# Kernel optimization log

Hardware: AMD Instinct MI355X
Metric: run time of the kernel (lower is better)

Reference implementation:

```python
import jax, jax.numpy as jnp
import numpy as np

D_STATE = 128   # Mamba2 default (the SS2D d_state=16 is never forwarded to Mamba2)
N_HEADS = 4     # d_ssm // headdim = d_model / (d_model//4)
D_CONV = 4
EPS = 1e-5


def silu(v):
    return v * jax.nn.sigmoid(v)


def setup_inputs() -> dict:
    key = jax.random.key(0)
    ks = jax.random.split(key, 12)
    d_model = 256
    d_inner = 2 * d_model            # expand=2
    d_ssm = d_model
    conv_dim = d_ssm + 2 * D_STATE   # 512
    d_in_proj = 2 * d_inner + 2 * D_STATE + N_HEADS  # 1284
    B, H, W = 8, 64, 64
    inp = {
        "x": jax.random.normal(ks[0], (B, d_model, H, W), jnp.float32),
        "in_proj_w": jax.random.normal(ks[1], (d_in_proj, d_model), jnp.float32) * 0.02,
        "conv_w": jax.random.normal(ks[2], (conv_dim, D_CONV), jnp.float32) * 0.2,
        "conv_b": jnp.zeros((conv_dim,), jnp.float32),
        "dt_bias": jax.random.normal(ks[3], (N_HEADS,), jnp.float32) * 0.1,
        "A_log": jnp.log(jax.random.uniform(ks[4], (N_HEADS,), jnp.float32, 1.0, 16.0)),
        "D": jax.random.normal(ks[5], (N_HEADS,), jnp.float32),
        "norm_w": jnp.ones((d_ssm,), jnp.float32),
        "out_proj_w": jax.random.normal(ks[6], (d_model, d_inner), jnp.float32) * 0.02,
        "se_w1": jax.random.normal(ks[7], (d_model // 4, d_model), jnp.float32) * 0.05,
        "se_b1": jnp.zeros((d_model // 4,), jnp.float32),
        "se_w2": jax.random.normal(ks[8], (d_model, d_model // 4), jnp.float32) * 0.05,
        "se_b2": jnp.zeros((d_model,), jnp.float32),
    }
    return inp


def _forward(x, in_proj_w, conv_w, conv_b, dt_bias, A_log, D, norm_w,
             out_proj_w, se_w1, se_b1, se_w2, se_b2):
    Bb, C, H, W = x.shape
    L = H * W
    d_model = C
    d_inner = 2 * d_model
    d_ssm = d_model
    d_mlp = d_inner - d_ssm
    headdim = d_ssm // N_HEADS
    conv_dim = d_ssm + 2 * D_STATE

    u = x.reshape(Bb, C, L).transpose(0, 2, 1)              # (b, l, c)
    zxbcdt = u @ in_proj_w.T                                 # (b, l, 1284)
    z0 = zxbcdt[..., :d_mlp]
    x0 = zxbcdt[..., d_mlp:2 * d_mlp]
    z = zxbcdt[..., 2 * d_mlp:2 * d_mlp + d_ssm]
    xBC = zxbcdt[..., 2 * d_mlp + d_ssm:2 * d_mlp + d_ssm + conv_dim]
    dt = zxbcdt[..., -N_HEADS:]

    dt = jax.nn.softplus(dt + dt_bias)                       # (b, l, h)

    # causal depthwise conv along l, kernel size D_CONV
    xpad = jnp.pad(xBC, ((0, 0), (D_CONV - 1, 0), (0, 0)))
    xconv = conv_b
    for k in range(D_CONV):
        xconv = xconv + xpad[:, k:k + L, :] * conv_w[:, k]
    xconv = silu(xconv)

    xs = xconv[..., :d_ssm]
    Bm = xconv[..., d_ssm:d_ssm + D_STATE]                   # (b, l, n) ngroups=1
    Cm = xconv[..., d_ssm + D_STATE:]                        # (b, l, n)
    xh = xs.reshape(Bb, L, N_HEADS, headdim)                 # (b, l, h, p)

    A = -jnp.exp(A_log)                                      # (h,)

    def step(hstate, inp):
        xt, dtt, Bt, Ct = inp  # (b,h,p), (b,h), (b,n), (b,n)
        dA = jnp.exp(dtt * A)                                # (b, h)
        hstate = hstate * dA[:, :, None, None] + \
            (dtt[:, :, None, None] * xt[..., None]) * Bt[:, None, None, :]
        y = jnp.einsum('bhpn,bn->bhp', hstate, Ct)
        return hstate, y

    h0 = jnp.zeros((Bb, N_HEADS, headdim, D_STATE), x.dtype)
    _, ys = jax.lax.scan(
        step, h0,
        (xh.transpose(1, 0, 2, 3), dt.transpose(1, 0, 2),
         Bm.transpose(1, 0, 2), Cm.transpose(1, 0, 2)))
    y = ys.transpose(1, 0, 2, 3)                             # (b, l, h, p)
    y = y + D[None, None, :, None] * xh                      # skip
    y = y.reshape(Bb, L, d_ssm)

    # gated RMSNorm (norm_before_gate=False): gate then normalize
    y = y * silu(z)
    y = y * jax.lax.rsqrt(jnp.mean(y * y, axis=-1, keepdims=True) + EPS) * norm_w

    y = jnp.concatenate([silu(z0) * x0, y], axis=-1)         # (b, l, d_inner)
    out = y @ out_proj_w.T                                   # (b, l, d_model)
    out = out.transpose(0, 2, 1).reshape(Bb, C, H, W)

    # SE-style spectral attention
    s = out.mean(axis=(2, 3))                                # (b, c)
    s = jax.nn.relu(s @ se_w1.T + se_b1)
    s = jax.nn.sigmoid(s @ se_w2.T + se_b2)
    return out * s[:, :, None, None]


def reference(x, in_proj_w, conv_w, conv_b, dt_bias, A_log, D, norm_w,
              out_proj_w, se_w1, se_b1, se_w2, se_b2):
    return _forward(x, in_proj_w, conv_w, conv_b, dt_bias, A_log, D, norm_w,
                    out_proj_w, se_w1, se_b1, se_w2, se_b2)
```

## Files before the change

### kernel.cpp

```cpp
#include <hip/hip_runtime.h>
#include <stdint.h>

typedef __attribute__((ext_vector_type(8))) short bf16x8;
typedef __attribute__((ext_vector_type(4))) float f32x4;

__device__ __forceinline__ float bf2f(unsigned short u) {
  unsigned int x = ((unsigned int)u) << 16;
  return __builtin_bit_cast(float, x);
}
__device__ __forceinline__ unsigned short f2bf(float f) {
  unsigned int x = __builtin_bit_cast(unsigned int, f);
  unsigned int r = x + 0x7FFFu + ((x >> 16) & 1u);
  return (unsigned short)(r >> 16);
}
__device__ __forceinline__ float silu(float v) { return v / (1.f + __expf(-v)); }
__device__ __forceinline__ f32x4 fz4() { f32x4 z; z[0]=0.f; z[1]=0.f; z[2]=0.f; z[3]=0.f; return z; }

#define LSEQ 4096
#define DMODEL 256
#define NIN 1284
#define NINP 1408

__global__ void k_prep_w(const float* __restrict__ w_in, const float* __restrict__ w_out,
                         unsigned short* __restrict__ wpad, unsigned short* __restrict__ woutbf) {
  int idx = blockIdx.x * 256 + threadIdx.x;
  const int tot1 = NINP * DMODEL;
  if (idx < tot1) {
    int n = idx / DMODEL, k = idx % DMODEL;
    int src = (n < 512) ? ((n & 1) ? 256 + (n >> 1) : (n >> 1)) : n;
    float v = (src < NIN) ? w_in[src * DMODEL + k] : 0.f;
    wpad[idx] = f2bf(v);
  } else {
    int j = idx - tot1;
    woutbf[j] = f2bf(w_out[j]);
  }
}

__global__ __launch_bounds__(256) void k_transpose_x(const float* __restrict__ x,
                                                     unsigned short* __restrict__ ubf) {
  __shared__ float t[64][65];
  int bid = blockIdx.x;
  int b = bid >> 8;
  int r = bid & 255;
  int lt = r >> 2, kt = r & 3;
  int l0 = lt * 64, k0 = kt * 64;
  int tid = threadIdx.x;
  int j = tid & 63, i0 = tid >> 6;
  for (int rr = 0; rr < 16; rr++) {
    int ki = i0 + rr * 4;
    t[ki][j] = x[(size_t)(b * DMODEL + k0 + ki) * LSEQ + l0 + j];
  }
  __syncthreads();
  for (int rr = 0; rr < 16; rr++) {
    int li = i0 + rr * 4;
    ubf[(size_t)(b * LSEQ + l0 + li) * DMODEL + k0 + j] = f2bf(t[j][li]);
  }
}

template <int KDIM, int LDA, int LDB, int EPI>
__global__ __launch_bounds__(256) void k_gemm(const unsigned short* __restrict__ A,
                                              const unsigned short* __restrict__ B,
                                              float* __restrict__ outF,
                                              unsigned short* __restrict__ outBF,
                                              unsigned short* __restrict__ outBF2,
                                              float* __restrict__ dtb, int tilesN) {
  __shared__ __align__(16) short lds[17408];
  short* As = lds;
  short* Bs = lds + 8192;
  int nwg = gridDim.x;
  int orig = blockIdx.x;
  int wgid = (nwg & 7) ? orig : ((orig & 7) * (nwg >> 3) + (orig >> 3));
  int tn = wgid % tilesN, tm = wgid / tilesN;
  int m0 = tm * 128, n0 = tn * 128;
  int tid = threadIdx.x;
  int w = tid >> 6, lane = tid & 63;
  int wr = w >> 1, wc = w & 1;
  f32x4 acc[4][4];
  for (int i = 0; i < 4; i++)
    for (int j = 0; j < 4; j++) acc[i][j] = fz4();

  for (int kt = 0; kt < KDIM / 64; kt++) {
    int k0 = kt * 64;
    for (int i = 0; i < 4; i++) {
      int rowblk = w * 32 + i * 8;
      int row = rowblk + (lane >> 3);
      int kc = (lane & 7) * 8;
      const unsigned short* ga = A + (size_t)(m0 + row) * LDA + k0 + kc;
      __builtin_amdgcn_global_load_lds((const __attribute__((address_space(1))) unsigned int*)ga,
                                       (__attribute__((address_space(3))) unsigned int*)&As[rowblk * 64],
                                       16, 0, 0);
      const unsigned short* gb = B + (size_t)(n0 + row) * LDB + k0 + kc;
      __builtin_amdgcn_global_load_lds((const __attribute__((address_space(1))) unsigned int*)gb,
                                       (__attribute__((address_space(3))) unsigned int*)&Bs[rowblk * 64],
                                       16, 0, 0);
    }
    __syncthreads();
    for (int kk = 0; kk < 64; kk += 32) {
      bf16x8 af[4], bfr[4];
      for (int mi = 0; mi < 4; mi++)
        af[mi] = *(const bf16x8*)&As[(wr * 64 + mi * 16 + (lane & 15)) * 64 + kk + (lane >> 4) * 8];
      for (int ni = 0; ni < 4; ni++)
        bfr[ni] = *(const bf16x8*)&Bs[(wc * 64 + ni * 16 + (lane & 15)) * 64 + kk + (lane >> 4) * 8];
      for (int mi = 0; mi < 4; mi++)
        for (int ni = 0; ni < 4; ni++)
          acc[mi][ni] = __builtin_amdgcn_mfma_f32_16x16x32_bf16(af[mi], bfr[ni], acc[mi][ni], 0, 0, 0);
    }
    __syncthreads();
  }

  int fq = lane >> 4, fr = lane & 15;
  if constexpr (EPI == 1) {
    float* Cf = (float*)lds;
    for (int ph = 0; ph < 2; ph++) {
      if (ph) __syncthreads();
      if (wc == ph) {
        for (int mi = 0; mi < 4; mi++)
          for (int ni = 0; ni < 4; ni++)
            for (int j = 0; j < 4; j++)
              Cf[(wr * 64 + mi * 16 + fq * 4 + j) * 68 + ni * 16 + fr] = acc[mi][ni][j];
      }
      __syncthreads();
      int rr = tid >> 4, cc = (tid & 15) * 4;
      for (int it = 0; it < 8; it++) {
        int r = it * 16 + rr;
        float4 v = *(const float4*)&Cf[r * 68 + cc];
        *(float4*)&outF[(size_t)(m0 + r) * 256 + n0 + ph * 64 + cc] = v;
      }
    }
  } else if constexpr (EPI == 2) {
    unsigned short* xbc = (unsigned short*)outF;
    if (n0 >= 1280) {
      if (wc == 0 && fr < 4) {
        for (int mi = 0; mi < 4; mi++)
          for (int j = 0; j < 4; j++) {
            int m = m0 + wr * 64 + mi * 16 + fq * 4 + j;
            dtb[m * 4 + fr] = acc[mi][0][j];
          }
      }
    } else if (n0 < 512) {
      short* Ct = lds;
      for (int mi = 0; mi < 4; mi++)
        for (int ni = 0; ni < 4; ni++)
          for (int j = 0; j < 4; j++) {
            float v = acc[mi][ni][j];
            float vp = __shfl_xor(v, 1, 64);
            if (!(fr & 1)) {
              float zc = silu(v) * vp;
              Ct[(wr * 64 + mi * 16 + fq * 4 + j) * 72 + wc * 32 + ni * 8 + (fr >> 1)] =
                  (short)f2bf(zc);
            }
          }
      __syncthreads();
      int r = tid >> 1, base = (tid & 1) * 32;
      for (int it = 0; it < 4; it++) {
        int cc = base + it * 8;
        uint4 v = *(const uint4*)&Ct[r * 72 + cc];
        *(uint4*)&outBF[(size_t)(m0 + r) * 512 + (n0 >> 1) + cc] = v;
      }
    } else {
      short* Ct = lds;
      for (int mi = 0; mi < 4; mi++)
        for (int ni = 0; ni < 4; ni++)
          for (int j = 0; j < 4; j++)
            Ct[(wr * 64 + mi * 16 + fq * 4 + j) * 136 + wc * 64 + ni * 16 + fr] =
                (short)f2bf(acc[mi][ni][j]);
      __syncthreads();
      int rr = tid >> 4, cc = (tid & 15) * 8;
      for (int it = 0; it < 8; it++) {
        int r = it * 16 + rr;
        uint4 v = *(const uint4*)&Ct[r * 136 + cc];
        if (n0 < 768) *(uint4*)&outBF2[(size_t)(m0 + r) * 256 + (n0 - 512) + cc] = v;
        else *(uint4*)&xbc[(size_t)(m0 + r) * 512 + (n0 - 768) + cc] = v;
      }
    }
  } else {
    bool dttile = (n0 >= 1280);
    if (dttile) {
      if (wc == 0 && fr < 4) {
        for (int mi = 0; mi < 4; mi++)
          for (int j = 0; j < 4; j++) {
            int m = m0 + wr * 64 + mi * 16 + fq * 4 + j;
            dtb[m * 4 + fr] = acc[mi][0][j];
          }
      }
    } else {
      short* Ct = lds;
      for (int mi = 0; mi < 4; mi++)
        for (int ni = 0; ni < 4; ni++)
          for (int j = 0; j < 4; j++)
            Ct[(wr * 64 + mi * 16 + fq * 4 + j) * 136 + wc * 64 + ni * 16 + fr] =
                (short)f2bf(acc[mi][ni][j]);
      __syncthreads();
      int rr = tid >> 4, cc = (tid & 15) * 8;
      for (int it = 0; it < 8; it++) {
        int r = it * 16 + rr;
        uint4 v = *(const uint4*)&Ct[r * 136 + cc];
        *(uint4*)&outBF[(size_t)(m0 + r) * 1280 + n0 + cc] = v;
      }
    }
  }
}

__global__ __launch_bounds__(256) void k_conv(const unsigned short* __restrict__ src, int stride,
                                              const float* __restrict__ conv_w,
                                              const float* __restrict__ conv_b,
                                              unsigned short* __restrict__ xs,
                                              unsigned short* __restrict__ bc,
                                              unsigned short* __restrict__ xsT,
                                              unsigned short* __restrict__ bT) {
  __shared__ __align__(16) unsigned short xt[35 * 512];
  int bid = blockIdx.x;
  int b = bid >> 7;
  int t0 = (bid & 127) * 32;
  int tid = threadIdx.x;
  for (int id = tid; id < 35 * 64; id += 256) {
    int r = id >> 6, ch = id & 63;
    int t = t0 - 3 + r;
    float4 v;
    if (t < 0) v = make_float4(0.f, 0.f, 0.f, 0.f);
    else v = *(const float4*)&src[(size_t)(b * LSEQ + t) * stride + ch * 8];
    *(float4*)&xt[r * 512 + ch * 8] = v;
  }
  __syncthreads();
  int c0 = tid, c1 = tid + 256;
  float w0[4], w1[4];
  for (int k = 0; k < 4; k++) { w0[k] = conv_w[c0 * 4 + k]; w1[k] = conv_w[c1 * 4 + k]; }
  float bb0 = conv_b[c0], bb1 = conv_b[c1];
  unsigned short xa0[32], xa1[32];
#pragma unroll
  for (int tl = 0; tl < 32; tl++) {
    float a0 = bb0, a1 = bb1;
    for (int k = 0; k < 4; k++) {
      a0 += bf2f(xt[(tl + k) * 512 + c0]) * w0[k];
      a1 += bf2f(xt[(tl + k) * 512 + c1]) * w1[k];
    }
    a0 = silu(a0); a1 = silu(a1);
    unsigned short u0 = f2bf(a0), u1 = f2bf(a1);
    xa0[tl] = u0; xa1[tl] = u1;
    size_t row = (size_t)(b * LSEQ + t0 + tl);
    xs[row * 256 + c0] = u0;
    bc[row * 256 + (c1 - 256)] = u1;
  }
  if (xsT) {
    const uint4* p0 = (const uint4*)xa0;
    for (int k = 0; k < 4; k++)
      *(uint4*)&xsT[((size_t)(b * 256 + c0)) * LSEQ + t0 + k * 8] = p0[k];
    if (c1 < 384) {
      const uint4* p1 = (const uint4*)xa1;
      for (int k = 0; k < 4; k++)
        *(uint4*)&bT[((size_t)(b * 128 + (c1 - 256))) * LSEQ + t0 + k * 8] = p1[k];
    }
  }
}

__global__ __launch_bounds__(256) void k_scan(const unsigned short* __restrict__ xs,
                                              const unsigned short* __restrict__ bc,
                                              const float* __restrict__ dtb,
                                              const float* __restrict__ dt_bias,
                                              const float* __restrict__ A_log,
                                              const float* __restrict__ Dp,
                                              unsigned short* __restrict__ y) {
  __shared__ __align__(16) unsigned short bcl[32 * 256];
  __shared__ float xsl[32][4];
  __shared__ float dtl[32], dal[32];
  int bid = blockIdx.x;
  int b = bid >> 6;
  int h = (bid >> 4) & 3;
  int pg = bid & 15;
  int tid = threadIdx.x, w = tid >> 6, lane = tid & 63;
  int p = pg * 4 + w;
  float Ah = -expf(A_log[h]);
  float Dh = Dp[h];
  float bias = dt_bias[h];
  float h0 = 0.f, h1 = 0.f;
  for (int t0 = 0; t0 < LSEQ; t0 += 32) {
    for (int id = tid; id < 32 * 32; id += 256) {
      int r = id >> 5, ch = id & 31;
      *(float4*)&bcl[r * 256 + ch * 8] =
          *(const float4*)&bc[(size_t)(b * LSEQ + t0 + r) * 256 + ch * 8];
    }
    if (tid < 128) {
      int r = tid >> 2, pp = tid & 3;
      xsl[r][pp] = bf2f(xs[(size_t)(b * LSEQ + t0 + r) * 256 + h * 64 + pg * 4 + pp]);
    } else if (tid < 160) {
      int r = tid - 128;
      float v = dtb[(size_t)(b * LSEQ + t0 + r) * 4 + h] + bias;
      float dt = (v > 20.f) ? v : log1pf(expf(v));
      dtl[r] = dt;
      dal[r] = expf(dt * Ah);
    }
    __syncthreads();
    for (int tl = 0; tl < 32; tl++) {
      float dtv = dtl[tl], dav = dal[tl], xv = xsl[tl][w];
      float bn  = bf2f(bcl[tl * 256 + lane]);
      float bn2 = bf2f(bcl[tl * 256 + 64 + lane]);
      float cn  = bf2f(bcl[tl * 256 + 128 + lane]);
      float cn2 = bf2f(bcl[tl * 256 + 192 + lane]);
      float coef = dtv * xv;
      h0 = h0 * dav + coef * bn;
      h1 = h1 * dav + coef * bn2;
      float part = h0 * cn + h1 * cn2;
      for (int off = 32; off; off >>= 1) part += __shfl_xor(part, off, 64);
      if (lane == 0)
        y[(size_t)(b * LSEQ + t0 + tl) * 256 + h * 64 + p] = f2bf(part + Dh * xv);
    }
    __syncthreads();
  }
}

__global__ __launch_bounds__(64) void k_dtpre(const float* __restrict__ dtraw,
                                              const float* __restrict__ dt_bias,
                                              const float* __restrict__ A_log,
                                              float* __restrict__ dts, float* __restrict__ cums) {
  int bid = blockIdx.x;
  int bh = bid >> 6, c = bid & 63;
  int b = bh >> 2, h = bh & 3;
  int lane = threadIdx.x;
  int t = c * 64 + lane;
  float v = dtraw[(size_t)(b * LSEQ + t) * 4 + h] + dt_bias[h];
  float dt = (v > 20.f) ? v : log1pf(expf(v));
  float Ah = -expf(A_log[h]);
  float s = dt * Ah;
  for (int off = 1; off < 64; off <<= 1) {
    float o = __shfl_up(s, off, 64);
    if (lane >= off) s += o;
  }
  dts[bh * LSEQ + t] = dt;
  cums[bh * LSEQ + t] = s;
}

__global__ __launch_bounds__(256) void k_chunkA(const unsigned short* __restrict__ bc,
                                                const unsigned short* __restrict__ xsT,
                                                const unsigned short* __restrict__ bT,
                                                const float* __restrict__ dts,
                                                const float* __restrict__ cums,
                                                float* __restrict__ ST,
                                                unsigned short* __restrict__ yb) {
  __shared__ __align__(16) unsigned short Bsm[64 * 128];
  __shared__ __align__(16) unsigned short BTs[128 * 64];
  __shared__ __align__(16) unsigned short XT[64 * 64];
  __shared__ __align__(16) unsigned short Ms[64 * 72];
  __shared__ float dtl[64], cuml[64], scl[64];
  int bid = blockIdx.x;
  int bh = bid >> 6, c = bid & 63;
  int b = bh >> 2, h = bh & 3;
  int m0 = b * LSEQ + c * 64;
  int tid = threadIdx.x, w = tid >> 6, lane = tid & 63;

  if (tid < 64) {
    dtl[tid] = dts[bh * LSEQ + c * 64 + tid];
    cuml[tid] = cums[bh * LSEQ + c * 64 + tid];
  }
  __syncthreads();
  float cumQ = cuml[63];

  for (int it = 0; it < 4; it++) {
    int idx = it * 256 + tid, row = idx >> 4, g = idx & 15;
    uint4 v = *(const uint4*)&bc[(size_t)(m0 + row) * 256 + g * 8];
    *(uint4*)((char*)Bsm + row * 256 + ((g ^ (row & 7)) << 4)) = v;
  }
  for (int it = 0; it < 2; it++) {
    int idx = it * 256 + tid, row = idx >> 3, g = idx & 7;
    uint4 v = *(const uint4*)&xsT[((size_t)(b * 256 + h * 64 + row)) * LSEQ + c * 64 + g * 8];
    *(uint4*)((char*)XT + row * 128 + ((g ^ (row & 7)) << 4)) = v;
  }
  if (tid < 64) scl[tid] = dtl[tid] * __expf(cumQ - cuml[tid]);
  __syncthreads();
  for (int it = 0; it < 4; it++) {
    int idx = it * 256 + tid, row = idx >> 3, g = idx & 7;
    uint4 v = *(const uint4*)&bT[((size_t)(b * 128 + row)) * LSEQ + c * 64 + g * 8];
    const unsigned short* pv = (const unsigned short*)&v;
    uint4 o; unsigned short* po = (unsigned short*)&o;
#pragma unroll
    for (int e = 0; e < 8; e++) po[e] = f2bf(bf2f(pv[e]) * scl[g * 8 + e]);
    *(uint4*)((char*)BTs + row * 128 + ((g ^ (row & 7)) << 4)) = o;
  }

  int rt = w * 16 + (lane & 15);
  const unsigned short* arow = bc + (size_t)(m0 + rt) * 256 + 128;
  f32x4 acc1[4];
#pragma unroll
  for (int i = 0; i < 4; i++) acc1[i] = fz4();
#pragma unroll
  for (int ks = 0; ks < 4; ks++) {
    int g = ks * 4 + (lane >> 4);
    bf16x8 a = *(const bf16x8*)&arow[g * 8];
#pragma unroll
    for (int ni = 0; ni < 4; ni++) {
      int rs = ni * 16 + (lane & 15);
      bf16x8 bfr = *(const bf16x8*)((char*)Bsm + rs * 256 + ((g ^ (rs & 7)) << 4));
      acc1[ni] = __builtin_amdgcn_mfma_f32_16x16x32_bf16(a, bfr, acc1[ni], 0, 0, 0);
    }
  }
#pragma unroll
  for (int ni = 0; ni < 4; ni++)
#pragma unroll
    for (int j = 0; j < 4; j++) {
      int t = w * 16 + (lane >> 4) * 4 + j;
      int s = ni * 16 + (lane & 15);
      float v = 0.f;
      if (t >= s) v = acc1[ni][j] * __expf(cuml[t] - cuml[s]) * dtl[s];
      *(unsigned short*)((char*)Ms + t * 128 + (((s >> 3) ^ (t & 7)) << 4) + ((s & 7) << 1)) = f2bf(v);
    }
  __syncthreads();

  f32x4 acc2[4], acc3[8];
#pragma unroll
  for (int i = 0; i < 4; i++) acc2[i] = fz4();
#pragma unroll
  for (int i = 0; i < 8; i++) acc3[i] = fz4();
#pragma unroll
  for (int ks = 0; ks < 2; ks++) {
    int g = ks * 4 + (lane >> 4);
    bf16x8 xf[4];
#pragma unroll
    for (int ni = 0; ni < 4; ni++) {
      int rp = ni * 16 + (lane & 15);
      xf[ni] = *(const bf16x8*)((char*)XT + rp * 128 + ((g ^ (rp & 7)) << 4));
    }
    {
      bf16x8 a = *(const bf16x8*)((char*)Ms + rt * 128 + ((g ^ (rt & 7)) << 4));
#pragma unroll
      for (int ni = 0; ni < 4; ni++)
        acc2[ni] = __builtin_amdgcn_mfma_f32_16x16x32_bf16(a, xf[ni], acc2[ni], 0, 0, 0);
    }
    {
      bf16x8 a3 = xf[w];
#pragma unroll
      for (int ni = 0; ni < 8; ni++) {
        int rn = ni * 16 + (lane & 15);
        bf16x8 bfr = *(const bf16x8*)((char*)BTs + rn * 128 + ((g ^ (rn & 7)) << 4));
        acc3[ni] = __builtin_amdgcn_mfma_f32_16x16x32_bf16(a3, bfr, acc3[ni], 0, 0, 0);
      }
    }
  }
  __syncthreads();
#pragma unroll
  for (int ni = 0; ni < 4; ni++)
#pragma unroll
    for (int j = 0; j < 4; j++) {
      int t = w * 16 + (lane >> 4) * 4 + j;
      int p = ni * 16 + (lane & 15);
      Ms[t * 72 + p] = f2bf(acc2[ni][j]);
    }
  float* stp = ST + ((size_t)bid << 13);
#pragma unroll
  for (int ni = 0; ni < 8; ni++)
#pragma unroll
    for (int j = 0; j < 4; j++) {
      int p = w * 16 + (lane >> 4) * 4 + j;
      int n = ni * 16 + (lane & 15);
      stp[p * 128 + n] = acc3[ni][j];
    }
  __syncthreads();
  {
    int rr = tid >> 3, cc = (tid & 7) * 8;
    for (int it = 0; it < 2; it++) {
      int t = it * 32 + rr;
      uint4 v = *(const uint4*)&Ms[t * 72 + cc];
      *(uint4*)&yb[(size_t)(m0 + t) * 256 + h * 64 + cc] = v;
    }
  }
}

__global__ __launch_bounds__(256) void k_chunkB(const float* __restrict__ ST,
                                                const float* __restrict__ cums,
                                                unsigned short* __restrict__ HT) {
  int bid = blockIdx.x;
  int bh = bid >> 3, psl = bid & 7;
  int p = psl * 8 + (threadIdx.x >> 5);
  int n0 = (threadIdx.x & 31) * 4;
  float H[4] = {0.f, 0.f, 0.f, 0.f};
  for (int c = 0; c < 64; c++) {
    size_t base = (size_t)(bh * 64 + c);
    ushort4 hv;
    unsigned short* ha = (unsigned short*)&hv;
#pragma unroll
    for (int e = 0; e < 4; e++) ha[e] = f2bf(H[e]);
    *(ushort4*)&HT[(base * 64 + p) * 128 + n0] = hv;
    float4 s4 = *(const float4*)&ST[(base << 13) + p * 128 + n0];
    float dec = __expf(cums[bh * LSEQ + c * 64 + 63]);
    H[0] = H[0] * dec + s4.x;
    H[1] = H[1] * dec + s4.y;
    H[2] = H[2] * dec + s4.z;
    H[3] = H[3] * dec + s4.w;
  }
}

__global__ __launch_bounds__(256) void k_chunkC(const unsigned short* __restrict__ bc,
                                                const unsigned short* __restrict__ xs,
                                                const unsigned short* __restrict__ HT,
                                                const float* __restrict__ cums,
                                                const float* __restrict__ Dp,
                                                unsigned short* __restrict__ yb) {
  __shared__ __align__(16) unsigned short Hs[64 * 128];
  __shared__ __align__(16) unsigned short yst[64 * 72];
  int bid = blockIdx.x;
  int bh = bid >> 6, c = bid & 63;
  int b = bh >> 2, h = bh & 3;
  int m0 = b * LSEQ + c * 64;
  int tid = threadIdx.x, w = tid >> 6, lane = tid & 63;
  float Dh = Dp[h];
  for (int it = 0; it < 4; it++) {
    int idx = it * 256 + tid, row = idx >> 4, g = idx & 15;
    uint4 v = *(const uint4*)&HT[((size_t)(bh * 64 + c) * 64 + row) * 128 + g * 8];
    *(uint4*)((char*)Hs + row * 256 + ((g ^ (row & 7)) << 4)) = v;
  }
  float exq[4];
  {
    int tb = w * 16 + (lane >> 4) * 4;
#pragma unroll
    for (int j = 0; j < 4; j++) exq[j] = __expf(cums[bh * LSEQ + c * 64 + tb + j]);
  }
  __syncthreads();
  int rt = w * 16 + (lane & 15);
  const unsigned short* arow = bc + (size_t)(m0 + rt) * 256 + 128;
  f32x4 acc[4];
#pragma unroll
  for (int i = 0; i < 4; i++) acc[i] = fz4();
#pragma unroll
  for (int ks = 0; ks < 4; ks++) {
    int g = ks * 4 + (lane >> 4);
    bf16x8 a = *(const bf16x8*)&arow[g * 8];
#pragma unroll
    for (int ni = 0; ni < 4; ni++) {
      int rp = ni * 16 + (lane & 15);
      bf16x8 bfr = *(const bf16x8*)((char*)Hs + rp * 256 + ((g ^ (rp & 7)) << 4));
      acc[ni] = __builtin_amdgcn_mfma_f32_16x16x32_bf16(a, bfr, acc[ni], 0, 0, 0);
    }
  }
#pragma unroll
  for (int ni = 0; ni < 4; ni++)
#pragma unroll
    for (int j = 0; j < 4; j++) {
      int t = w * 16 + (lane >> 4) * 4 + j;
      int p = ni * 16 + (lane & 15);
      yst[t * 72 + p] = f2bf(acc[ni][j] * exq[j]);
    }
  __syncthreads();
  {
    int rr = tid >> 3, cc = (tid & 7) * 8;
    for (int it = 0; it < 2; it++) {
      int t = it * 32 + rr;
      size_t off = (size_t)(m0 + t) * 256 + h * 64 + cc;
      uint4 yo = *(const uint4*)&yb[off];
      uint4 xv = *(const uint4*)&xs[off];
      const unsigned short* pyo = (const unsigned short*)&yo;
      const unsigned short* pxv = (const unsigned short*)&xv;
      const unsigned short* pys = &yst[t * 72 + cc];
      uint4 vo;
      unsigned short* po = (unsigned short*)&vo;
#pragma unroll
      for (int e = 0; e < 8; e++)
        po[e] = f2bf(bf2f(pyo[e]) + bf2f(pys[e]) + Dh * bf2f(pxv[e]));
      *(uint4*)&yb[off] = vo;
    }
  }
}

template <int MODE>
__global__ __launch_bounds__(256) void k_ycat(const unsigned short* __restrict__ y,
                                              const unsigned short* __restrict__ zsrc,
                                              const float* __restrict__ norm_w,
                                              unsigned short* __restrict__ ocat) {
  int bid = blockIdx.x;
  int tid = threadIdx.x, w = tid >> 6, lane = tid & 63;
  size_t m = (size_t)bid * 4 + w;
  int j0 = lane * 4;
  ushort4 yv = *(const ushort4*)&y[m * 256 + j0];
  ushort4 zv;
  if constexpr (MODE == 0) zv = *(const ushort4*)&zsrc[m * 256 + j0];
  else zv = *(const ushort4*)&zsrc[m * 1280 + 512 + j0];
  unsigned short ya[4] = {yv.x, yv.y, yv.z, yv.w};
  unsigned short za[4] = {zv.x, zv.y, zv.z, zv.w};
  float g[4]; float ssum = 0.f;
  for (int i = 0; i < 4; i++) {
    float gg = bf2f(ya[i]) * silu(bf2f(za[i]));
    g[i] = gg; ssum += gg * gg;
  }
  for (int off = 32; off; off >>= 1) ssum += __shfl_xor(ssum, off, 64);
  float inv = rsqrtf(ssum * (1.f / 256.f) + 1e-5f);
  ushort4 o2;
  unsigned short* o2a = (unsigned short*)&o2;
  for (int i = 0; i < 4; i++) o2a[i] = f2bf(g[i] * norm_w[j0 + i] * inv);
  *(ushort4*)&ocat[m * 512 + 256 + j0] = o2;
  if constexpr (MODE == 1) {
    ushort4 p0 = *(const ushort4*)&zsrc[m * 1280 + 2 * j0];
    ushort4 p1 = *(const ushort4*)&zsrc[m * 1280 + 2 * j0 + 4];
    ushort4 o1;
    unsigned short* o1a = (unsigned short*)&o1;
    o1a[0] = f2bf(silu(bf2f(p0.x)) * bf2f(p0.y));
    o1a[1] = f2bf(silu(bf2f(p0.z)) * bf2f(p0.w));
    o1a[2] = f2bf(silu(bf2f(p1.x)) * bf2f(p1.y));
    o1a[3] = f2bf(silu(bf2f(p1.z)) * bf2f(p1.w));
    *(ushort4*)&ocat[m * 512 + j0] = o1;
  }
}

__global__ void k_zero(float* __restrict__ p) { p[blockIdx.x * 256 + threadIdx.x] = 0.f; }

__global__ __launch_bounds__(256) void k_semean(const float* __restrict__ res, float* __restrict__ smean) {
  int bid = blockIdx.x;
  int b = bid >> 5, ch = bid & 31;
  int c = threadIdx.x;
  float acc = 0.f;
  for (int r = 0; r < 128; r++)
    acc += res[(size_t)(b * LSEQ + ch * 128 + r) * 256 + c];
  atomicAdd(&smean[b * 256 + c], acc);
}

__global__ __launch_bounds__(512) void k_sefc(const float* __restrict__ smean,
                                              const float* __restrict__ w1, const float* __restrict__ b1,
                                              const float* __restrict__ w2, const float* __restrict__ b2,
                                              float* __restrict__ s2) {
  __shared__ float s1[512];
  int tid = threadIdx.x;
  int b = tid >> 6, j = tid & 63;
  float acc = b1[j];
  for (int k = 0; k < 256; k++) acc += smean[b * 256 + k] * (1.f / 4096.f) * w1[j * 256 + k];
  s1[b * 64 + j] = fmaxf(acc, 0.f);
  __syncthreads();
  for (int idx = tid; idx < 2048; idx += 512) {
    int bb = idx >> 8, c = idx & 255;
    float a2 = b2[c];
    for (int k = 0; k < 64; k++) a2 += s1[bb * 64 + k] * w2[c * 64 + k];
    s2[idx] = 1.f / (1.f + expf(-a2));
  }
}

__global__ __launch_bounds__(256) void k_final(const float* __restrict__ res,
                                               const float* __restrict__ s2,
                                               float* __restrict__ out) {
  __shared__ float t[64][65];
  int bid = blockIdx.x;
  int b = bid >> 8;
  int r = bid & 255;
  int ct = r >> 6, lt = r & 63;
  int c0 = ct * 64, l0 = lt * 64;
  int tid = threadIdx.x, j = tid & 63, i0 = tid >> 6;
  for (int rr = 0; rr < 16; rr++) {
    int i = i0 + rr * 4;
    t[i][j] = res[(size_t)(b * LSEQ + l0 + i) * 256 + c0 + j];
  }
  __syncthreads();
  for (int rr = 0; rr < 16; rr++) {
    int ci = i0 + rr * 4;
    float s = s2[b * 256 + c0 + ci];
    out[(size_t)(b * 256 + c0 + ci) * LSEQ + l0 + j] = t[j][ci] * s;
  }
}

extern "C" void kernel_launch(void* const* d_in, const int* in_sizes, int n_in,
                              void* d_out, int out_size, void* d_ws, size_t ws_size,
                              hipStream_t stream) {
  const float* x         = (const float*)d_in[0];
  const float* in_proj_w = (const float*)d_in[1];
  const float* conv_w    = (const float*)d_in[2];
  const float* conv_b    = (const float*)d_in[3];
  const float* dt_bias   = (const float*)d_in[4];
  const float* A_log     = (const float*)d_in[5];
  const float* Dp        = (const float*)d_in[6];
  const float* norm_w    = (const float*)d_in[7];
  const float* out_projw = (const float*)d_in[8];
  const float* se_w1     = (const float*)d_in[9];
  const float* se_b1     = (const float*)d_in[10];
  const float* se_w2     = (const float*)d_in[11];
  const float* se_b2     = (const float*)d_in[12];
  float* out = (float*)d_out;
  char* ws = (char*)d_ws;

  const size_t NEED_CHUNKED = 220676096;

  if (ws_size >= NEED_CHUNKED) {
    float*          ST    = (float*)(ws + 0);
    unsigned short* ubf   = (unsigned short*)(ws + 0);
    unsigned short* xbc   = (unsigned short*)(ws + 16777216);
    float*          res   = (float*)(ws + 0);
    unsigned short* zcat  = (unsigned short*)(ws + 67108864);
    unsigned short* zbuf  = (unsigned short*)(ws + 100663296);
    unsigned short* xsb   = (unsigned short*)(ws + 117440512);
    unsigned short* bcb   = (unsigned short*)(ws + 134217728);
    unsigned short* HT    = (unsigned short*)(ws + 150994944);
    unsigned short* xsT   = (unsigned short*)(ws + 150994944);
    unsigned short* bT    = (unsigned short*)(ws + 167772160);
    unsigned short* ybuf  = (unsigned short*)(ws + 184549376);
    unsigned short* wpad  = (unsigned short*)(ws + 201326592);
    unsigned short* woutb = (unsigned short*)(ws + 202047488);
    float*          dtraw = (float*)(ws + 202309632);
    float*          dts   = (float*)(ws + 202833920);
    float*          cums  = (float*)(ws + 203358208);
    float*          smean = (float*)(ws + 203882496);
    float*          s2    = (float*)(ws + 203890688);

    k_prep_w<<<1920, 256, 0, stream>>>(in_proj_w, out_projw, wpad, woutb);
    k_transpose_x<<<2048, 256, 0, stream>>>(x, ubf);
    k_gemm<256, 256, 256, 2><<<256 * 11, 256, 0, stream>>>(ubf, wpad, (float*)xbc, zcat, zbuf, dtraw, 11);
    k_conv<<<1024, 256, 0, stream>>>(xbc, 512, conv_w, conv_b, xsb, bcb, xsT, bT);
    k_dtpre<<<2048, 64, 0, stream>>>(dtraw, dt_bias, A_log, dts, cums);
    k_chunkA<<<2048, 256, 0, stream>>>(bcb, xsT, bT, dts, cums, ST, ybuf);
    k_chunkB<<<256, 256, 0, stream>>>(ST, cums, HT);
    k_chunkC<<<2048, 256, 0, stream>>>(bcb, xsb, HT, cums, Dp, ybuf);
    k_ycat<0><<<8192, 256, 0, stream>>>(ybuf, zbuf, norm_w, zcat);
    k_gemm<512, 512, 512, 1><<<256 * 2, 256, 0, stream>>>(zcat, woutb, res, nullptr, nullptr, nullptr, 2);
    k_zero<<<8, 256, 0, stream>>>(smean);
    k_semean<<<256, 256, 0, stream>>>(res, smean);
    k_sefc<<<1, 512, 0, stream>>>(smean, se_w1, se_b1, se_w2, se_b2, s2);
    k_final<<<2048, 256, 0, stream>>>(res, s2, out);
  } else {
    unsigned short* ubf   = (unsigned short*)(ws + 0);
    unsigned short* xsb   = (unsigned short*)(ws + 16777216);
    float*          res   = (float*)(ws + 0);
    unsigned short* bcb   = (unsigned short*)(ws + 33554432);
    unsigned short* zx    = (unsigned short*)(ws + 50331648);
    float*          dtb   = (float*)(ws + 134217728);
    unsigned short* ybuf  = (unsigned short*)(ws + 134742016);
    unsigned short* ycat  = (unsigned short*)(ws + 151519232);
    unsigned short* wpad  = (unsigned short*)(ws + 185073664);
    unsigned short* woutb = (unsigned short*)(ws + 185794560);
    float*          smean = (float*)(ws + 186056704);
    float*          s2    = (float*)(ws + 186064896);

    k_prep_w<<<1920, 256, 0, stream>>>(in_proj_w, out_projw, wpad, woutb);
    k_transpose_x<<<2048, 256, 0, stream>>>(x, ubf);
    k_gemm<256, 256, 256, 0><<<256 * 11, 256, 0, stream>>>(ubf, wpad, nullptr, zx, nullptr, dtb, 11);
    k_conv<<<1024, 256, 0, stream>>>(zx + 768, 1280, conv_w, conv_b, xsb, bcb, nullptr, nullptr);
    k_scan<<<512, 256, 0, stream>>>(xsb, bcb, dtb, dt_bias, A_log, Dp, ybuf);
    k_ycat<1><<<8192, 256, 0, stream>>>(ybuf, zx, norm_w, ycat);
    k_gemm<512, 512, 512, 1><<<256 * 2, 256, 0, stream>>>(ycat, woutb, res, nullptr, nullptr, nullptr, 2);
    k_zero<<<8, 256, 0, stream>>>(smean);
    k_semean<<<256, 256, 0, stream>>>(res, smean);
    k_sefc<<<1, 512, 0, stream>>>(smean, se_w1, se_b1, se_w2, se_b2, s2);
    k_final<<<2048, 256, 0, stream>>>(res, s2, out);
  }
}
```

Baseline: 236.1 us.

## Merge prep kernels, fold dt precompute into conv, XOR-swizzle GEMM LDS tiles

```diff
diff --git a/kernel.cpp b/kernel.cpp
--- a/kernel.cpp
+++ b/kernel.cpp
@@ -21,30 +21,33 @@
 #define NIN 1284
 #define NINP 1408
 
-__global__ void k_prep_w(const float* __restrict__ w_in, const float* __restrict__ w_out,
-                         unsigned short* __restrict__ wpad, unsigned short* __restrict__ woutbf) {
-  int idx = blockIdx.x * 256 + threadIdx.x;
-  const int tot1 = NINP * DMODEL;
-  if (idx < tot1) {
-    int n = idx / DMODEL, k = idx % DMODEL;
-    int src = (n < 512) ? ((n & 1) ? 256 + (n >> 1) : (n >> 1)) : n;
-    float v = (src < NIN) ? w_in[src * DMODEL + k] : 0.f;
-    wpad[idx] = f2bf(v);
-  } else {
-    int j = idx - tot1;
-    woutbf[j] = f2bf(w_out[j]);
-  }
-}
-
-__global__ __launch_bounds__(256) void k_transpose_x(const float* __restrict__ x,
-                                                     unsigned short* __restrict__ ubf) {
+__global__ __launch_bounds__(256) void k_prep(const float* __restrict__ w_in,
+                                              const float* __restrict__ w_out,
+                                              unsigned short* __restrict__ wpad,
+                                              unsigned short* __restrict__ woutbf,
+                                              const float* __restrict__ x,
+                                              unsigned short* __restrict__ ubf) {
+  int bid = blockIdx.x;
+  int tid = threadIdx.x;
+  if (bid < 1920) {
+    int idx = bid * 256 + tid;
+    const int tot1 = NINP * DMODEL;
+    if (idx < tot1) {
+      int n = idx / DMODEL, k = idx % DMODEL;
+      int src = (n < 512) ? ((n & 1) ? 256 + (n >> 1) : (n >> 1)) : n;
+      float v = (src < NIN) ? w_in[src * DMODEL + k] : 0.f;
+      wpad[idx] = f2bf(v);
+    } else {
+      int j = idx - tot1;
+      woutbf[j] = f2bf(w_out[j]);
+    }
+    return;
+  }
   __shared__ float t[64][65];
-  int bid = blockIdx.x;
-  int b = bid >> 8;
-  int r = bid & 255;
+  int r = (bid - 1920) & 255;
+  int b = (bid - 1920) >> 8;
   int lt = r >> 2, kt = r & 3;
   int l0 = lt * 64, k0 = kt * 64;
-  int tid = threadIdx.x;
   int j = tid & 63, i0 = tid >> 6;
   for (int rr = 0; rr < 16; rr++) {
     int ki = i0 + rr * 4;
@@ -84,7 +87,7 @@
     for (int i = 0; i < 4; i++) {
       int rowblk = w * 32 + i * 8;
       int row = rowblk + (lane >> 3);
-      int kc = (lane & 7) * 8;
+      int kc = ((lane & 7) ^ (row & 7)) * 8;
       const unsigned short* ga = A + (size_t)(m0 + row) * LDA + k0 + kc;
       __builtin_amdgcn_global_load_lds((const __attribute__((address_space(1))) unsigned int*)ga,
                                        (__attribute__((address_space(3))) unsigned int*)&As[rowblk * 64],
@@ -96,11 +99,16 @@
     }
     __syncthreads();
     for (int kk = 0; kk < 64; kk += 32) {
+      int gq = (kk >> 3) + (lane >> 4);
       bf16x8 af[4], bfr[4];
-      for (int mi = 0; mi < 4; mi++)
-        af[mi] = *(const bf16x8*)&As[(wr * 64 + mi * 16 + (lane & 15)) * 64 + kk + (lane >> 4) * 8];
-      for (int ni = 0; ni < 4; ni++)
-        bfr[ni] = *(const bf16x8*)&Bs[(wc * 64 + ni * 16 + (lane & 15)) * 64 + kk + (lane >> 4) * 8];
+      for (int mi = 0; mi < 4; mi++) {
+        int rt = wr * 64 + mi * 16 + (lane & 15);
+        af[mi] = *(const bf16x8*)((const char*)As + rt * 128 + ((gq ^ (rt & 7)) << 4));
+      }
+      for (int ni = 0; ni < 4; ni++) {
+        int rs = wc * 64 + ni * 16 + (lane & 15);
+        bfr[ni] = *(const bf16x8*)((const char*)Bs + rs * 128 + ((gq ^ (rs & 7)) << 4));
+      }
       for (int mi = 0; mi < 4; mi++)
         for (int ni = 0; ni < 4; ni++)
           acc[mi][ni] = __builtin_amdgcn_mfma_f32_16x16x32_bf16(af[mi], bfr[ni], acc[mi][ni], 0, 0, 0);
@@ -207,12 +215,35 @@
                                               unsigned short* __restrict__ xs,
                                               unsigned short* __restrict__ bc,
                                               unsigned short* __restrict__ xsT,
-                                              unsigned short* __restrict__ bT) {
+                                              unsigned short* __restrict__ bT,
+                                              const float* __restrict__ dtraw,
+                                              const float* __restrict__ dt_bias,
+                                              const float* __restrict__ A_log,
+                                              float* __restrict__ dts,
+                                              float* __restrict__ cums) {
   __shared__ __align__(16) unsigned short xt[35 * 512];
   int bid = blockIdx.x;
+  int tid = threadIdx.x;
+  if (bid >= 1024) {
+    int w4 = tid >> 6, lane = tid & 63;
+    int gc = (bid - 1024) * 4 + w4;
+    int bh = gc >> 6, cc = gc & 63;
+    int b2 = bh >> 2, h2 = bh & 3;
+    int t = cc * 64 + lane;
+    float v = dtraw[(size_t)(b2 * LSEQ + t) * 4 + h2] + dt_bias[h2];
+    float dt = (v > 20.f) ? v : log1pf(__expf(v));
+    float Ah = -__expf(A_log[h2]);
+    float s = dt * Ah;
+    for (int off = 1; off < 64; off <<= 1) {
+      float o = __shfl_up(s, off, 64);
+      if (lane >= off) s += o;
+    }
+    dts[bh * LSEQ + t] = dt;
+    cums[bh * LSEQ + t] = s;
+    return;
+  }
   int b = bid >> 7;
   int t0 = (bid & 127) * 32;
-  int tid = threadIdx.x;
   for (int id = tid; id < 35 * 64; id += 256) {
     int r = id >> 6, ch = id & 63;
     int t = t0 - 3 + r;
@@ -306,27 +337,6 @@
     }
     __syncthreads();
   }
-}
-
-__global__ __launch_bounds__(64) void k_dtpre(const float* __restrict__ dtraw,
-                                              const float* __restrict__ dt_bias,
-                                              const float* __restrict__ A_log,
-                                              float* __restrict__ dts, float* __restrict__ cums) {
-  int bid = blockIdx.x;
-  int bh = bid >> 6, c = bid & 63;
-  int b = bh >> 2, h = bh & 3;
-  int lane = threadIdx.x;
-  int t = c * 64 + lane;
-  float v = dtraw[(size_t)(b * LSEQ + t) * 4 + h] + dt_bias[h];
-  float dt = (v > 20.f) ? v : log1pf(expf(v));
-  float Ah = -expf(A_log[h]);
-  float s = dt * Ah;
-  for (int off = 1; off < 64; off <<= 1) {
-    float o = __shfl_up(s, off, 64);
-    if (lane >= off) s += o;
-  }
-  dts[bh * LSEQ + t] = dt;
-  cums[bh * LSEQ + t] = s;
 }
 
 __global__ __launch_bounds__(256) void k_chunkA(const unsigned short* __restrict__ bc,
@@ -692,11 +702,10 @@
     float*          smean = (float*)(ws + 203882496);
     float*          s2    = (float*)(ws + 203890688);
 
-    k_prep_w<<<1920, 256, 0, stream>>>(in_proj_w, out_projw, wpad, woutb);
-    k_transpose_x<<<2048, 256, 0, stream>>>(x, ubf);
+    k_prep<<<3968, 256, 0, stream>>>(in_proj_w, out_projw, wpad, woutb, x, ubf);
     k_gemm<256, 256, 256, 2><<<256 * 11, 256, 0, stream>>>(ubf, wpad, (float*)xbc, zcat, zbuf, dtraw, 11);
-    k_conv<<<1024, 256, 0, stream>>>(xbc, 512, conv_w, conv_b, xsb, bcb, xsT, bT);
-    k_dtpre<<<2048, 64, 0, stream>>>(dtraw, dt_bias, A_log, dts, cums);
+    k_conv<<<1536, 256, 0, stream>>>(xbc, 512, conv_w, conv_b, xsb, bcb, xsT, bT,
+                                     dtraw, dt_bias, A_log, dts, cums);
     k_chunkA<<<2048, 256, 0, stream>>>(bcb, xsT, bT, dts, cums, ST, ybuf);
     k_chunkB<<<256, 256, 0, stream>>>(ST, cums, HT);
     k_chunkC<<<2048, 256, 0, stream>>>(bcb, xsb, HT, cums, Dp, ybuf);
@@ -720,10 +729,10 @@
     float*          smean = (float*)(ws + 186056704);
     float*          s2    = (float*)(ws + 186064896);
 
-    k_prep_w<<<1920, 256, 0, stream>>>(in_proj_w, out_projw, wpad, woutb);
-    k_transpose_x<<<2048, 256, 0, stream>>>(x, ubf);
+    k_prep<<<3968, 256, 0, stream>>>(in_proj_w, out_projw, wpad, woutb, x, ubf);
     k_gemm<256, 256, 256, 0><<<256 * 11, 256, 0, stream>>>(ubf, wpad, nullptr, zx, nullptr, dtb, 11);
-    k_conv<<<1024, 256, 0, stream>>>(zx + 768, 1280, conv_w, conv_b, xsb, bcb, nullptr, nullptr);
+    k_conv<<<1024, 256, 0, stream>>>(zx + 768, 1280, conv_w, conv_b, xsb, bcb, nullptr, nullptr,
+                                     nullptr, nullptr, nullptr, nullptr, nullptr);
     k_scan<<<512, 256, 0, stream>>>(xsb, bcb, dtb, dt_bias, A_log, Dp, ybuf);
     k_ycat<1><<<8192, 256, 0, stream>>>(ybuf, zx, norm_w, ycat);
     k_gemm<512, 512, 512, 1><<<256 * 2, 256, 0, stream>>>(ycat, woutb, res, nullptr, nullptr, nullptr, 2);
```

Result: faster. 226.3 us (-4.2%).
